# Kernel optimization log

Hardware: AMD Instinct MI355X
Metric: run time of the kernel (lower is better)

Reference implementation:

```python
import jax, jax.numpy as jnp
import numpy as np
from jax import lax

B, IN_CH, OUT_CH, K, STYLE_DIM, H, W = 4, 512, 512, 3, 512, 64, 64


def setup_inputs() -> dict:
    key = jax.random.key(0)
    ks = jax.random.split(key, 6)
    x = jax.random.normal(ks[0], (B, B * IN_CH, H, W), dtype=jnp.float32)
    style = jax.random.normal(ks[1], (B, STYLE_DIM), dtype=jnp.float32)
    # learned params
    weight = jax.random.normal(ks[2], (1, OUT_CH, IN_CH, K, K), dtype=jnp.float32)
    demod = jnp.ones((1, OUT_CH, 1, 1), dtype=jnp.float32)
    # nn.Linear(style_dim, in_channels): kaiming-uniform-ish init approximated
    lim = 1.0 / np.sqrt(STYLE_DIM)
    mod_w = jax.random.uniform(ks[3], (IN_CH, STYLE_DIM), minval=-lim, maxval=lim, dtype=jnp.float32)
    mod_b = jax.random.uniform(ks[4], (IN_CH,), minval=-lim, maxval=lim, dtype=jnp.float32)
    return {"x": x, "style": style, "weight": weight, "demod": demod, "mod_w": mod_w, "mod_b": mod_b}


def reference(x, style, weight, demod, mod_w, mod_b):
    b = x.shape[0]
    out_ch, in_ch, k = weight.shape[1], weight.shape[2], weight.shape[3]
    # style modulation: Linear(style) -> (B, in_ch) -> (B,1,in_ch,1,1)
    s = style @ mod_w.T + mod_b
    w = weight * s[:, None, :, None, None]          # (B, out, in, k, k)
    # demod (1,out,1,1) broadcasts against trailing (in,k,k) axes -> needs out==in (as in torch)
    w = w * demod
    w = w.reshape(b * out_ch, in_ch, k, k)           # OIHW grouped kernel
    pad = k // 2
    out = lax.conv_general_dilated(
        x, w,
        window_strides=(1, 1),
        padding=[(pad, pad), (pad, pad)],
        dimension_numbers=("NCHW", "OIHW", "NCHW"),
        feature_group_count=b,
    )
    return out  # (B, B*out_ch, H, W)
```

## Files before the change

kernel.cpp:

```cpp
#include <hip/hip_runtime.h>

typedef __attribute__((ext_vector_type(4))) float f32x4;
typedef __attribute__((ext_vector_type(16))) float f32x16;
typedef __attribute__((ext_vector_type(8))) short bf16x8;
typedef unsigned long long u64;
typedef unsigned short u16;
typedef unsigned int u32;

static __device__ __forceinline__ u16 f2bf(float f) {
    u32 u = __float_as_uint(f);
    u += 0x7fffu + ((u >> 16) & 1u);
    return (u16)(u >> 16);
}

__global__ void k_style(const float* __restrict__ style, const float* __restrict__ mod_w,
                        const float* __restrict__ mod_b, float* __restrict__ s_ws) {
    int t = blockIdx.x * 256 + threadIdx.x;
    int g = t >> 9, ic = t & 511;
    const f32x4* st = (const f32x4*)(style + (g << 9));
    const f32x4* mw = (const f32x4*)(mod_w + (ic << 9));
    float acc = 0.f;
#pragma unroll 4
    for (int d = 0; d < 128; ++d) {
        f32x4 a = st[d], b = mw[d];
        acc += a[0]*b[0] + a[1]*b[1] + a[2]*b[2] + a[3]*b[3];
    }
    s_ws[t] = acc + mod_b[ic];
}

__global__ void k_wmod(const float* __restrict__ weight, const float* __restrict__ demod,
                       const float* __restrict__ s_ws, short* __restrict__ wmod) {
    int t = blockIdx.x * 256 + threadIdx.x;
    int lane = t & 63; int r = t >> 6;
    int oh = r & 1; r >>= 1;
    int kk = r & 1; r >>= 1;
    int ch = r & 15; r >>= 4;
    int wr = r & 1; r >>= 1;
    int ocb = r & 3;
    int oc  = ocb*128 + wr*64 + oh*32 + (lane & 31);
    int ic0 = ch*32 + kk*16 + (lane >> 5)*8;
    const float* wp = weight + (size_t)(oc*512 + ic0)*9;
    float wv[8][9];
#pragma unroll
    for (int e = 0; e < 8; ++e)
#pragma unroll
        for (int tp = 0; tp < 9; ++tp) wv[e][tp] = wp[e*9 + tp];
    float dm[8];
#pragma unroll
    for (int e = 0; e < 8; ++e) dm[e] = demod[ic0 + e];
#pragma unroll 1
    for (int g = 0; g < 4; ++g) {
        float sv[8];
#pragma unroll
        for (int e = 0; e < 8; ++e) sv[e] = s_ws[(g << 9) + ic0 + e] * dm[e];
        short* base = wmod + ((size_t)((g*4 + ocb)*2 + wr)) * 294912
                    + (((kk << 1) + oh) << 9) + (lane << 3);
#pragma unroll
        for (int tp = 0; tp < 9; ++tp) {
            bf16x8 pk;
#pragma unroll
            for (int e = 0; e < 8; ++e) pk[e] = (short)f2bf(wv[e][tp] * sv[e]);
            *(bf16x8*)&base[(size_t)(ch*9 + tp) << 11] = pk;
        }
    }
}

__global__ __launch_bounds__(256) void k_xcast(const float* __restrict__ x,
                                               short* __restrict__ xb) {
    __shared__ short Ls[64 * 520];
    const int tid = threadIdx.x;
    const int y = blockIdx.x, g = blockIdx.y, nb = blockIdx.z;
    const float* src = x + (((size_t)(nb * 2048 + (g << 9))) << 12) + (y << 6);
#pragma unroll
    for (int it = 0; it < 32; ++it) {
        int j = it * 256 + tid;
        int ic = j >> 4, p4 = j & 15;
        f32x4 v = *(const f32x4*)(src + ((size_t)ic << 12) + (p4 << 2));
        int kk = (ic >> 3) & 3;
        int fb = (ic >> 5) * 32 + (ic & 7);
#pragma unroll
        for (int c = 0; c < 4; ++c) {
            int px = (p4 << 2) + c;
            int k = kk ^ ((px >> 1) & 3);
            Ls[px * 520 + fb + k * 8] = (short)f2bf(v[c]);
        }
    }
    __syncthreads();
    short* dstb = xb + ((size_t)((nb * 4 + g) * 64 + y) << 15);
#pragma unroll
    for (int it = 0; it < 16; ++it) {
        int j = it * 256 + tid;
        int ch = j >> 8, px = (j >> 2) & 63, k = j & 3;
        *(bf16x8*)&dstb[(size_t)j << 3] = *(const bf16x8*)&Ls[px * 520 + ch * 32 + k * 8];
    }
}

__global__ __launch_bounds__(256, 4) void k_conv(const short* __restrict__ xb,
                                                 const short* __restrict__ wmod,
                                                 float* __restrict__ out) {
    __shared__ __align__(16) short Xs[2 * 8448];

    const int tid  = threadIdx.x;
    const int lane = tid & 63;
    const int wv   = tid >> 6;
    const int wr   = wv >> 1, wc = wv & 1;
    const int l31  = lane & 31;
    const int lh   = lane >> 5;
    const int ocb  = blockIdx.x & 3, rowb = blockIdx.x >> 2;
    const int g    = blockIdx.y, nb = blockIdx.z;
    const int y0   = rowb << 1;

    const short* xbg = xb + ((size_t)((nb * 4 + g) * 64) << 15);
    const short* wg  = wmod + ((size_t)((g * 4 + ocb) * 2 + wr)) * 294912;
    float* outg = out + (((size_t)(nb * 2048 + (g << 9) + ocb * 128)) << 12) + (rowb << 7);

    const int gy = y0 - 1 + wv;
    const bool srow = (gy >= 0 && gy <= 63);
    const short* xsrc = xbg + ((size_t)(srow ? gy : 0) << 15) + (lane << 3);
    short* xdst0 = Xs + ((wv * 66 + 1) << 5);

    const short* wp = wg + (lane << 3);

    for (int i = tid; i < 4224; i += 256) ((u64*)Xs)[i] = 0ull;

    f32x16 acc[2][2];
#pragma unroll
    for (int oh = 0; oh < 2; ++oh)
#pragma unroll
        for (int ph = 0; ph < 2; ++ph)
#pragma unroll
            for (int r = 0; r < 16; ++r) acc[oh][ph][r] = 0.f;

    __syncthreads();

    if (srow) {
#pragma unroll
        for (int q = 0; q < 4; ++q)
            __builtin_amdgcn_global_load_lds(
                (const __attribute__((address_space(1))) void*)(xsrc + (q << 9)),
                (__attribute__((address_space(3))) void*)(xdst0 + (q << 9)), 16, 0, 0);
    }
    __builtin_amdgcn_sched_barrier(0);
    bf16x8 na0 = *(const bf16x8*)(wp);
    bf16x8 na1 = *(const bf16x8*)(wp + 512);
    bf16x8 na2 = *(const bf16x8*)(wp + 1024);
    bf16x8 na3 = *(const bf16x8*)(wp + 1536);
    wp += 2048;

#pragma unroll 1
    for (int ch = 0; ch < 16; ++ch) {
        asm volatile("s_waitcnt vmcnt(4)" ::: "memory");
        __builtin_amdgcn_s_barrier();
        __builtin_amdgcn_sched_barrier(0);
        if (ch < 15 && srow) {
            const short* s = xsrc + ((size_t)(ch + 1) << 11);
            short* d = xdst0 + (((ch + 1) & 1) ? 8448 : 0);
#pragma unroll
            for (int q = 0; q < 4; ++q)
                __builtin_amdgcn_global_load_lds(
                    (const __attribute__((address_space(1))) void*)(s + (q << 9)),
                    (__attribute__((address_space(3))) void*)(d + (q << 9)), 16, 0, 0);
        }
        __builtin_amdgcn_sched_barrier(0);
        const int bb = (ch & 1) * 8448;

        int pB[3];
#pragma unroll
        for (int d = 0; d < 3; ++d) {
            const int xr = l31 + d - 1;
            pB[d] = bb + ((wc * 66 + 1 + xr) << 5) + ((lh ^ ((xr >> 1) & 3)) << 3);
        }

#pragma unroll
        for (int tap = 0; tap < 9; ++tap) {
            bf16x8 ca0 = na0, ca1 = na1, ca2 = na2, ca3 = na3;
            na0 = *(const bf16x8*)(wp);
            na1 = *(const bf16x8*)(wp + 512);
            na2 = *(const bf16x8*)(wp + 1024);
            na3 = *(const bf16x8*)(wp + 1536);
            wp += 2048;

            const int p0 = pB[tap % 3] + (tap / 3) * 2112;
            const int p1 = p0 ^ 16;
            bf16x8 b00 = *(const bf16x8*)&Xs[p0];
            bf16x8 b01 = *(const bf16x8*)&Xs[p0 + 1024];
            bf16x8 b10 = *(const bf16x8*)&Xs[p1];
            bf16x8 b11 = *(const bf16x8*)&Xs[p1 + 1024];

            __builtin_amdgcn_s_setprio(1);
            acc[0][0] = __builtin_amdgcn_mfma_f32_32x32x16_bf16(ca0, b00, acc[0][0], 0, 0, 0);
            acc[0][1] = __builtin_amdgcn_mfma_f32_32x32x16_bf16(ca0, b01, acc[0][1], 0, 0, 0);
            acc[1][0] = __builtin_amdgcn_mfma_f32_32x32x16_bf16(ca1, b00, acc[1][0], 0, 0, 0);
            acc[1][1] = __builtin_amdgcn_mfma_f32_32x32x16_bf16(ca1, b01, acc[1][1], 0, 0, 0);
            acc[0][0] = __builtin_amdgcn_mfma_f32_32x32x16_bf16(ca2, b10, acc[0][0], 0, 0, 0);
            acc[0][1] = __builtin_amdgcn_mfma_f32_32x32x16_bf16(ca2, b11, acc[0][1], 0, 0, 0);
            acc[1][0] = __builtin_amdgcn_mfma_f32_32x32x16_bf16(ca3, b10, acc[1][0], 0, 0, 0);
            acc[1][1] = __builtin_amdgcn_mfma_f32_32x32x16_bf16(ca3, b11, acc[1][1], 0, 0, 0);
            __builtin_amdgcn_s_setprio(0);
        }
    }

#pragma unroll
    for (int oh = 0; oh < 2; ++oh)
#pragma unroll
        for (int ph = 0; ph < 2; ++ph) {
            float* dst = outg + ((size_t)((wr << 6) + (oh << 5) + (lh << 2)) << 12)
                       + (wc << 6) + (ph << 5) + l31;
#pragma unroll
            for (int r = 0; r < 16; ++r)
                dst[(size_t)(((r & 3) + ((r >> 2) << 3)) << 12)] = acc[oh][ph][r];
        }
}

extern "C" void kernel_launch(void* const* d_in, const int* in_sizes, int n_in,
                              void* d_out, int out_size, void* d_ws, size_t ws_size,
                              hipStream_t stream) {
    const float* x      = (const float*)d_in[0];
    const float* style  = (const float*)d_in[1];
    const float* weight = (const float*)d_in[2];
    const float* demod  = (const float*)d_in[3];
    const float* mod_w  = (const float*)d_in[4];
    const float* mod_b  = (const float*)d_in[5];
    float* out = (float*)d_out;

    float* s_ws = (float*)d_ws;
    short* wmod = (short*)((char*)d_ws + 8192);
    short* xbuf = (short*)((char*)d_ws + 8192 + 18874368);

    hipLaunchKernelGGL(k_style, dim3(8), dim3(256), 0, stream, style, mod_w, mod_b, s_ws);
    hipLaunchKernelGGL(k_wmod, dim3(128), dim3(256), 0, stream, weight, demod, s_ws, wmod);
    hipLaunchKernelGGL(k_xcast, dim3(64, 4, 4), dim3(256), 0, stream, x, xbuf);
    hipLaunchKernelGGL(k_conv, dim3(128, 4, 4), dim3(256), 0, stream, xbuf, wmod, out);
}
```

Measured before the change: 370.6 us.

## Parallelize weight modulation and input cast, reorder conv block mapping

Result: faster. 360.9 us (-2.6%).

```diff
diff --git a/kernel.cpp b/kernel.cpp
--- a/kernel.cpp
+++ b/kernel.cpp
@@ -36,66 +36,40 @@
     int kk = r & 1; r >>= 1;
     int ch = r & 15; r >>= 4;
     int wr = r & 1; r >>= 1;
-    int ocb = r & 3;
+    int ocb = r & 3; r >>= 2;
+    int g = r & 3;
     int oc  = ocb*128 + wr*64 + oh*32 + (lane & 31);
     int ic0 = ch*32 + kk*16 + (lane >> 5)*8;
     const float* wp = weight + (size_t)(oc*512 + ic0)*9;
-    float wv[8][9];
-#pragma unroll
-    for (int e = 0; e < 8; ++e)
-#pragma unroll
-        for (int tp = 0; tp < 9; ++tp) wv[e][tp] = wp[e*9 + tp];
-    float dm[8];
-#pragma unroll
-    for (int e = 0; e < 8; ++e) dm[e] = demod[ic0 + e];
-#pragma unroll 1
-    for (int g = 0; g < 4; ++g) {
-        float sv[8];
-#pragma unroll
-        for (int e = 0; e < 8; ++e) sv[e] = s_ws[(g << 9) + ic0 + e] * dm[e];
-        short* base = wmod + ((size_t)((g*4 + ocb)*2 + wr)) * 294912
-                    + (((kk << 1) + oh) << 9) + (lane << 3);
-#pragma unroll
-        for (int tp = 0; tp < 9; ++tp) {
-            bf16x8 pk;
-#pragma unroll
-            for (int e = 0; e < 8; ++e) pk[e] = (short)f2bf(wv[e][tp] * sv[e]);
-            *(bf16x8*)&base[(size_t)(ch*9 + tp) << 11] = pk;
-        }
+    float sv[8];
+#pragma unroll
+    for (int e = 0; e < 8; ++e) sv[e] = s_ws[(g << 9) + ic0 + e] * demod[ic0 + e];
+    short* base = wmod + ((size_t)((g*4 + ocb)*2 + wr)) * 294912
+                + (((kk << 1) + oh) << 9) + (lane << 3);
+#pragma unroll
+    for (int tp = 0; tp < 9; ++tp) {
+        bf16x8 pk;
+#pragma unroll
+        for (int e = 0; e < 8; ++e) pk[e] = (short)f2bf(wp[e*9 + tp] * sv[e]);
+        *(bf16x8*)&base[(size_t)(ch*9 + tp) << 11] = pk;
     }
 }
 
 __global__ __launch_bounds__(256) void k_xcast(const float* __restrict__ x,
                                                short* __restrict__ xb) {
-    __shared__ short Ls[64 * 520];
-    const int tid = threadIdx.x;
-    const int y = blockIdx.x, g = blockIdx.y, nb = blockIdx.z;
-    const float* src = x + (((size_t)(nb * 2048 + (g << 9))) << 12) + (y << 6);
-#pragma unroll
-    for (int it = 0; it < 32; ++it) {
-        int j = it * 256 + tid;
-        int ic = j >> 4, p4 = j & 15;
-        f32x4 v = *(const f32x4*)(src + ((size_t)ic << 12) + (p4 << 2));
-        int kk = (ic >> 3) & 3;
-        int fb = (ic >> 5) * 32 + (ic & 7);
-#pragma unroll
-        for (int c = 0; c < 4; ++c) {
-            int px = (p4 << 2) + c;
-            int k = kk ^ ((px >> 1) & 3);
-            Ls[px * 520 + fb + k * 8] = (short)f2bf(v[c]);
-        }
-    }
-    __syncthreads();
-    short* dstb = xb + ((size_t)((nb * 4 + g) * 64 + y) << 15);
-#pragma unroll
-    for (int it = 0; it < 16; ++it) {
-        int j = it * 256 + tid;
-        int ch = j >> 8, px = (j >> 2) & 63, k = j & 3;
-        *(bf16x8*)&dstb[(size_t)j << 3] = *(const bf16x8*)&Ls[px * 520 + ch * 32 + k * 8];
-    }
-}
-
-__global__ __launch_bounds__(256, 4) void k_conv(const short* __restrict__ xb,
+    int o = blockIdx.x * 256 + threadIdx.x;
+    int k  = o & 3, px = (o >> 2) & 63, ch = (o >> 8) & 15;
+    int y  = (o >> 12) & 63, g = (o >> 18) & 3, nb = o >> 20;
+    int ic0 = ch * 32 + ((k ^ ((px >> 1) & 3)) << 3);
+    const float* src = x + (((size_t)(nb * 2048 + (g << 9) + ic0)) << 12) + (y << 6) + px;
+    bf16x8 pk;
+#pragma unroll
+    for (int e = 0; e < 8; ++e)
+        pk[e] = (short)f2bf(src[(size_t)e << 12]);
+    ((bf16x8*)xb)[o] = pk;
+}
+
+__global__ __launch_bounds__(256, 3) void k_conv(const short* __restrict__ xb,
                                                  const short* __restrict__ wmod,
                                                  float* __restrict__ out) {
     __shared__ __align__(16) short Xs[2 * 8448];
@@ -106,7 +80,7 @@
     const int wr   = wv >> 1, wc = wv & 1;
     const int l31  = lane & 31;
     const int lh   = lane >> 5;
-    const int ocb  = blockIdx.x & 3, rowb = blockIdx.x >> 2;
+    const int ocb  = blockIdx.x >> 5, rowb = blockIdx.x & 31;
     const int g    = blockIdx.y, nb = blockIdx.z;
     const int y0   = rowb << 1;
 
@@ -228,7 +202,7 @@
     short* xbuf = (short*)((char*)d_ws + 8192 + 18874368);
 
     hipLaunchKernelGGL(k_style, dim3(8), dim3(256), 0, stream, style, mod_w, mod_b, s_ws);
-    hipLaunchKernelGGL(k_wmod, dim3(128), dim3(256), 0, stream, weight, demod, s_ws, wmod);
-    hipLaunchKernelGGL(k_xcast, dim3(64, 4, 4), dim3(256), 0, stream, x, xbuf);
+    hipLaunchKernelGGL(k_wmod, dim3(1024), dim3(256), 0, stream, weight, demod, s_ws, wmod);
+    hipLaunchKernelGGL(k_xcast, dim3(16384), dim3(256), 0, stream, x, xbuf);
     hipLaunchKernelGGL(k_conv, dim3(128, 4, 4), dim3(256), 0, stream, xbuf, wmod, out);
 }
```
